# Performance work log

Hardware: AMD Instinct MI355X
Metric: run time of the kernel (lower is better)

The kernel has to match this reference:

```python
import jax, jax.numpy as jnp
import numpy as np

N_NODES = 50000
NUM_HYPEREDGES = 50000


def setup_inputs() -> dict:
    key = jax.random.key(0)
    k1, k2, k3, k4, k5 = jax.random.split(key, 5)
    E = 1_600_000
    F_IN, F_OUT = 128, 128
    X = jax.random.normal(k1, (N_NODES, F_IN), dtype=jnp.float32)
    nodes = jax.random.randint(k2, (E,), 0, N_NODES, dtype=jnp.int64)
    hedges = jax.random.randint(k3, (E,), 0, NUM_HYPEREDGES, dtype=jnp.int64)
    edge_index = jnp.stack([nodes, hedges], axis=0)
    W = jax.random.normal(k4, (F_IN, F_OUT), dtype=jnp.float32) * (1.0 / np.sqrt(F_IN))
    b = jax.random.normal(k5, (F_OUT,), dtype=jnp.float32) * 0.02
    return {"X": X, "edge_index": edge_index, "W": W, "b": b}


def reference(X, edge_index, W, b):
    nodes = edge_index[0]   # [E] node ids (source of incidence)
    hedges = edge_index[1]  # [E] hyperedge ids
    ones = jnp.ones(nodes.shape[0], dtype=X.dtype)

    # x = lin(X)  (Linear, bias=False inside conv)
    x = X @ W  # [N, F_out]

    # B = 1 / hyperedge degree (inf -> 0)
    deg_e = jax.ops.segment_sum(ones, hedges, num_segments=NUM_HYPEREDGES)
    B_inv = jnp.where(deg_e > 0, 1.0 / deg_e, 0.0)

    # D = 1 / node degree (unit hyperedge weights; inf -> 0)
    deg_v = jax.ops.segment_sum(ones, nodes, num_segments=N_NODES)
    D_inv = jnp.where(deg_v > 0, 1.0 / deg_v, 0.0)

    # node -> hyperedge aggregation: m_e = B_e * sum_{v in e} x_v
    m = jax.ops.segment_sum(x[nodes], hedges, num_segments=NUM_HYPEREDGES)
    m = m * B_inv[:, None]  # [M, F_out]

    # hyperedge -> node aggregation: out_v = D_v * sum_{e ni v} m_e
    out = jax.ops.segment_sum(m[hedges], nodes, num_segments=N_NODES)
    out = out * D_inv[:, None] + b  # [N, F_out]

    return jax.nn.softmax(out, axis=1)
```

## Files before the change

### kernel.cpp

```cpp
#include <hip/hip_runtime.h>
#include <hip/hip_fp16.h>

#define NN 50000
#define NM 50000
#define F  128
#define NBUK 782
#define CHSZ 8192
typedef unsigned short ushort_t;
typedef _Float16 f16;
typedef f16 f16x8 __attribute__((ext_vector_type(8)));
typedef float f32x4 __attribute__((ext_vector_type(4)));

union HF4 { float4 f4; __half2 h2[4]; };
union PK4 { uint2 u2; f16 h[4]; };

__device__ __forceinline__ int wscan64(int v, int lane) {
    int x = v;
#pragma unroll
    for (int s = 1; s < 64; s <<= 1) {
        int u = __shfl_up(x, s, 64);
        if (lane >= s) x += u;
    }
    return x;
}

__device__ __forceinline__ int bscan256(int v, int* s5, int* tot) {
    int t = threadIdx.x, lane = t & 63, wid = t >> 6;
    int incl = wscan64(v, lane);
    if (lane == 63) s5[wid] = incl;
    __syncthreads();
    if (t == 0) {
        int a = 0;
#pragma unroll
        for (int j = 0; j < 4; ++j) { int x = s5[j]; s5[j] = a; a += x; }
        s5[4] = a;
    }
    __syncthreads();
    int ex = incl - v + s5[wid];
    *tot = s5[4];
    __syncthreads();
    return ex;
}

__global__ __launch_bounds__(256) void wprep_k(const float* __restrict__ W,
                                               f16* __restrict__ Wt) {
    int i = blockIdx.x * 256 + threadIdx.x;
    int k = i >> 7, c = i & 127;
    Wt[c * 128 + k] = (f16)W[i];
}

struct GemmSmem { f16 sXh[64 * 128]; };
struct SortSmem { int hist[NBUK]; int cursor[NBUK]; int pairs[CHSZ]; int s5[5]; };
union alignas(16) FatSmem { GemmSmem g; SortSmem s; };

__global__ __launch_bounds__(256) void fat_k(const float* __restrict__ X,
                                             const f16* __restrict__ Wt,
                                             f16* __restrict__ xh,
                                             const int* __restrict__ nodes,
                                             const int* __restrict__ hedges,
                                             int* __restrict__ gchunk0, int* __restrict__ gchunk1,
                                             int* __restrict__ ghist, int* __restrict__ gstart,
                                             int E, int NCH, int nsort) {
    __shared__ FatSmem u;
    int t = threadIdx.x;

    if ((int)blockIdx.x < nsort) {
        int dir = blockIdx.x / NCH;
        int c   = blockIdx.x % NCH;
        const int* key = dir ? nodes  : hedges;
        const int* pay = dir ? hedges : nodes;
        int* gchunk    = dir ? gchunk1 : gchunk0;
        int e0 = c * CHSZ, e1 = min(E, e0 + CHSZ);

        for (int i = t; i < NBUK; i += 256) u.s.hist[i] = 0;
        __syncthreads();
        for (int e = e0 + t; e < e1; e += 256) atomicAdd(&u.s.hist[key[e] >> 6], 1);
        __syncthreads();

        int carry = 0;
        for (int base = 0; base < NBUK; base += 256) {
            int i = base + t;
            int v = (i < NBUK) ? u.s.hist[i] : 0;
            int tot;
            int ex = bscan256(v, u.s.s5, &tot);
            if (i < NBUK) u.s.cursor[i] = ex + carry;
            carry += tot;
        }
        __syncthreads();

        for (int b = t; b < NBUK; b += 256) {
            size_t idx = ((size_t)dir * NBUK + b) * NCH + c;
            ghist[idx]  = u.s.hist[b];
            gstart[idx] = u.s.cursor[b];
        }
        __syncthreads();

        for (int e = e0 + t; e < e1; e += 256) {
            int k = key[e];
            int pos = atomicAdd(&u.s.cursor[k >> 6], 1);
            u.s.pairs[pos] = ((k & 63) << 16) | pay[e];
        }
        __syncthreads();

        int n = e1 - e0;
        for (int i = t; i < n; i += 256) gchunk[(size_t)c * CHSZ + i] = u.s.pairs[i];
    } else {
        int gb = blockIdx.x - nsort;
        int row0 = gb * 64;

        const float4* X4 = (const float4*)X;
        for (int i = t; i < 64 * 32; i += 256) {
            int r = i >> 5, cq = i & 31;
            int gr = row0 + r;
            float4 xv = (gr < NN) ? X4[(size_t)gr * 32 + cq]
                                  : make_float4(0.f, 0.f, 0.f, 0.f);
            PK4 pk;
            pk.h[0] = (f16)xv.x; pk.h[1] = (f16)xv.y;
            pk.h[2] = (f16)xv.z; pk.h[3] = (f16)xv.w;
            int byte = (r * 256 + cq * 8) ^ ((r & 7) << 4);
            *(uint2*)((char*)u.g.sXh + byte) = pk.u2;
        }
        __syncthreads();

        int l = t & 63, w = t >> 6;
        int lr = l & 15, lk = l >> 4;
        f32x4 acc[8];
#pragma unroll
        for (int c = 0; c < 8; ++c) acc[c] = (f32x4){0.f, 0.f, 0.f, 0.f};

#pragma unroll
        for (int ks = 0; ks < 4; ++ks) {
            int rloc = w * 16 + lr;
            int abyte = (rloc * 256 + ks * 64 + lk * 16) ^ ((rloc & 7) << 4);
            f16x8 afrag = *(const f16x8*)((const char*)u.g.sXh + abyte);
#pragma unroll
            for (int c = 0; c < 8; ++c) {
                f16x8 bfrag = *(const f16x8*)(Wt + (c * 16 + lr) * 128 + ks * 32 + lk * 8);
                acc[c] = __builtin_amdgcn_mfma_f32_16x16x32_f16(afrag, bfrag, acc[c], 0, 0, 0);
            }
        }

#pragma unroll
        for (int c = 0; c < 8; ++c) {
            int col = c * 16 + lr;
#pragma unroll
            for (int j = 0; j < 4; ++j) {
                int row = row0 + w * 16 + lk * 4 + j;
                if (row < NN) xh[(size_t)row * 128 + col] = (f16)acc[c][j];
            }
        }
    }
}

__global__ __launch_bounds__(256) void rowsum_k(const int* __restrict__ ghist,
                                                int* __restrict__ bsum, int NCH) {
    int row = blockIdx.x * 4 + (threadIdx.x >> 6);
    int l = threadIdx.x & 63;
    if (row >= 2 * NBUK) return;
    const int* r = ghist + (size_t)row * NCH;
    int s = 0;
    for (int c = l; c < NCH; c += 64) s += r[c];
#pragma unroll
    for (int k = 32; k >= 1; k >>= 1) s += __shfl_xor(s, k, 64);
    if (l == 0) bsum[row] = s;
}

__global__ __launch_bounds__(1024) void bucketbase_k(const int* __restrict__ bsum,
                                                     int* __restrict__ bstart,
                                                     int* __restrict__ off0, int* __restrict__ off1,
                                                     int E) {
    __shared__ int s16[17];
    int dir = blockIdx.x;
    int t = threadIdx.x, lane = t & 63, wid = t >> 6;
    int v = (t < NBUK) ? bsum[dir * NBUK + t] : 0;
    int incl = wscan64(v, lane);
    if (lane == 63) s16[wid] = incl;
    __syncthreads();
    if (t < 16) {
        int x = s16[t], y = x;
#pragma unroll
        for (int s = 1; s < 16; s <<= 1) {
            int u = __shfl_up(y, s, 64);
            if (t >= s) y += u;
        }
        s16[t] = y - x;
    }
    __syncthreads();
    int ex = incl - v + s16[wid];
    if (t < NBUK) bstart[dir * NBUK + t] = ex;
    if (t == 0) (dir ? off1 : off0)[50000] = E;
}

__global__ __launch_bounds__(256) void merge_scatter_k(const int* __restrict__ gchunk0, const int* __restrict__ gchunk1,
                                                       const int* __restrict__ ghist, const int* __restrict__ gstart,
                                                       const int* __restrict__ bstart,
                                                       ushort_t* __restrict__ adj0, ushort_t* __restrict__ adj1,
                                                       int* __restrict__ off0, int* __restrict__ off1,
                                                       int NCH) {
    __shared__ int ssrc[256];
    __shared__ int sdst[257];
    __shared__ int s5[5];
    __shared__ int pairsS[CHSZ];
    __shared__ int fcnt[64], foff[64], fcur[64];

    int dir = blockIdx.x / NBUK;
    int b   = blockIdx.x % NBUK;
    int t   = threadIdx.x;
    const int* gchunk   = dir ? gchunk1 : gchunk0;
    ushort_t* adj       = dir ? adj1 : adj0;
    int* offD           = dir ? off1 : off0;

    int len = 0, src = 0;
    if (t < NCH) {
        size_t idx = ((size_t)dir * NBUK + b) * NCH + t;
        len = ghist[idx];
        src = gstart[idx];
    }
    ssrc[t] = src;
    int tot;
    int ex = bscan256(len, s5, &tot);
    sdst[t] = ex;
    if (t == 0) sdst[256] = 0x7FFFFFFF;
    if (t < 64) fcnt[t] = 0;
    __syncthreads();
    int T = tot;

    int per = (T + 255) >> 8;
    int i0 = t * per, i1 = min(T, i0 + per);
    if (i0 < i1) {
        int lo = 0, hi = 255;
        while (lo < hi) {
            int mid = (lo + hi + 1) >> 1;
            if (sdst[mid] <= i0) lo = mid; else hi = mid - 1;
        }
        int c = lo;
        for (int i = i0; i < i1; ++i) {
            while (c < 255 && sdst[c + 1] <= i) ++c;
            int p = gchunk[(size_t)c * CHSZ + ssrc[c] + (i - sdst[c])];
            pairsS[i] = p;
            atomicAdd(&fcnt[p >> 16], 1);
        }
    }
    __syncthreads();

    int bst = bstart[dir * NBUK + b];
    if (t < 64) {
        int x = fcnt[t];
        int y = wscan64(x, t);
        foff[t] = y - x;
        fcur[t] = y - x;
        int d = b * 64 + t;
        if (d < 50000) offD[d] = bst + foff[t];
    }
    __syncthreads();

    for (int i = t; i < T; i += 256) {
        int p = pairsS[i];
        int slot = atomicAdd(&fcur[p >> 16], 1);
        adj[(size_t)bst + slot] = (ushort_t)(p & 0xFFFF);
    }
}

__global__ __launch_bounds__(256) void agg_a_k(const float4* __restrict__ x4,
                                               const ushort_t* __restrict__ adj,
                                               const int* __restrict__ off,
                                               float4* __restrict__ m4) {
    int t = threadIdx.x;
    int seg = blockIdx.x * 4 + (t >> 6);
    int l = t & 63;
    int rg = l >> 4, cc = l & 15;
    int p0 = off[seg], p1 = off[seg + 1];
    float acc[8] = {};
    int i = p0;
    for (; i + 16 <= p1; i += 16) {
        int r0 = adj[i + rg], r1 = adj[i + 4 + rg], r2 = adj[i + 8 + rg], r3 = adj[i + 12 + rg];
        HF4 u0, u1, u2, u3;
        u0.f4 = x4[(size_t)r0 * 16 + cc];
        u1.f4 = x4[(size_t)r1 * 16 + cc];
        u2.f4 = x4[(size_t)r2 * 16 + cc];
        u3.f4 = x4[(size_t)r3 * 16 + cc];
#pragma unroll
        for (int k = 0; k < 4; ++k) {
            float2 f0 = __half22float2(u0.h2[k]);
            float2 f1 = __half22float2(u1.h2[k]);
            float2 f2 = __half22float2(u2.h2[k]);
            float2 f3 = __half22float2(u3.h2[k]);
            acc[2 * k]     += (f0.x + f1.x) + (f2.x + f3.x);
            acc[2 * k + 1] += (f0.y + f1.y) + (f2.y + f3.y);
        }
    }
    for (; i < p1; i += 4) {
        int r = i + rg;
        if (r < p1) {
            HF4 u;
            u.f4 = x4[(size_t)adj[r] * 16 + cc];
#pragma unroll
            for (int k = 0; k < 4; ++k) {
                float2 f = __half22float2(u.h2[k]);
                acc[2 * k] += f.x; acc[2 * k + 1] += f.y;
            }
        }
    }
#pragma unroll
    for (int k = 0; k < 8; ++k) {
        acc[k] += __shfl_xor(acc[k], 16, 64);
        acc[k] += __shfl_xor(acc[k], 32, 64);
    }
    if (l < 16) {
        float inv = (p1 > p0) ? 1.0f / (float)(p1 - p0) : 0.0f;
        HF4 w;
#pragma unroll
        for (int k = 0; k < 4; ++k)
            w.h2[k] = __floats2half2_rn(acc[2 * k] * inv, acc[2 * k + 1] * inv);
        m4[(size_t)seg * 16 + cc] = w.f4;
    }
}

__global__ __launch_bounds__(256) void agg_b_k(const float4* __restrict__ m4,
                                               const ushort_t* __restrict__ adj,
                                               const int* __restrict__ off,
                                               const float* __restrict__ bias,
                                               float4* __restrict__ out4) {
    int t = threadIdx.x;
    int seg = blockIdx.x * 4 + (t >> 6);
    int l = t & 63;
    int rg = l >> 4, cc = l & 15;
    int p0 = off[seg], p1 = off[seg + 1];
    float acc[8] = {};
    int i = p0;
    for (; i + 16 <= p1; i += 16) {
        int r0 = adj[i + rg], r1 = adj[i + 4 + rg], r2 = adj[i + 8 + rg], r3 = adj[i + 12 + rg];
        HF4 u0, u1, u2, u3;
        u0.f4 = m4[(size_t)r0 * 16 + cc];
        u1.f4 = m4[(size_t)r1 * 16 + cc];
        u2.f4 = m4[(size_t)r2 * 16 + cc];
        u3.f4 = m4[(size_t)r3 * 16 + cc];
#pragma unroll
        for (int k = 0; k < 4; ++k) {
            float2 f0 = __half22float2(u0.h2[k]);
            float2 f1 = __half22float2(u1.h2[k]);
            float2 f2 = __half22float2(u2.h2[k]);
            float2 f3 = __half22float2(u3.h2[k]);
            acc[2 * k]     += (f0.x + f1.x) + (f2.x + f3.x);
            acc[2 * k + 1] += (f0.y + f1.y) + (f2.y + f3.y);
        }
    }
    for (; i < p1; i += 4) {
        int r = i + rg;
        if (r < p1) {
            HF4 u;
            u.f4 = m4[(size_t)adj[r] * 16 + cc];
#pragma unroll
            for (int k = 0; k < 4; ++k) {
                float2 f = __half22float2(u.h2[k]);
                acc[2 * k] += f.x; acc[2 * k + 1] += f.y;
            }
        }
    }
#pragma unroll
    for (int k = 0; k < 8; ++k) {
        acc[k] += __shfl_xor(acc[k], 16, 64);
        acc[k] += __shfl_xor(acc[k], 32, 64);
    }
    float inv = (p1 > p0) ? 1.0f / (float)(p1 - p0) : 0.0f;
    const float4* b4 = (const float4*)bias;
    float4 bb0 = b4[cc * 2], bb1 = b4[cc * 2 + 1];
    float lg[8];
    lg[0] = acc[0] * inv + bb0.x; lg[1] = acc[1] * inv + bb0.y;
    lg[2] = acc[2] * inv + bb0.z; lg[3] = acc[3] * inv + bb0.w;
    lg[4] = acc[4] * inv + bb1.x; lg[5] = acc[5] * inv + bb1.y;
    lg[6] = acc[6] * inv + bb1.z; lg[7] = acc[7] * inv + bb1.w;

    float mx = lg[0];
#pragma unroll
    for (int k = 1; k < 8; ++k) mx = fmaxf(mx, lg[k]);
#pragma unroll
    for (int s = 1; s < 16; s <<= 1) mx = fmaxf(mx, __shfl_xor(mx, s, 16));
    float e[8], sm = 0.f;
#pragma unroll
    for (int k = 0; k < 8; ++k) { e[k] = __expf(lg[k] - mx); sm += e[k]; }
#pragma unroll
    for (int s = 1; s < 16; s <<= 1) sm += __shfl_xor(sm, s, 16);
    float r = 1.0f / sm;
    if (l < 16) {
        out4[(size_t)seg * 32 + cc * 2]     = make_float4(e[0] * r, e[1] * r, e[2] * r, e[3] * r);
        out4[(size_t)seg * 32 + cc * 2 + 1] = make_float4(e[4] * r, e[5] * r, e[6] * r, e[7] * r);
    }
}

extern "C" void kernel_launch(void* const* d_in, const int* in_sizes, int n_in,
                              void* d_out, int out_size, void* d_ws, size_t ws_size,
                              hipStream_t stream) {
    const float* X  = (const float*)d_in[0];
    const int*   ei = (const int*)d_in[1];
    const float* W  = (const float*)d_in[2];
    const float* b  = (const float*)d_in[3];

    int E = in_sizes[1] / 2;
    const int* nodes  = ei;
    const int* hedges = ei + E;
    int NCH = (E + CHSZ - 1) / CHSZ;
    int nsort = 2 * NCH;
    int gemmb = (NN + 63) / 64;

    char* p = (char*)d_ws;
    f16* xh = (f16*)p;                    p += (size_t)NN * F * 2;
    f16* mh = (f16*)p;                    p += (size_t)NM * F * 2;
    ushort_t* adj0 = (ushort_t*)p;        p += (size_t)E * 2;
    ushort_t* adj1 = (ushort_t*)p;        p += (size_t)E * 2;
    int* ghist  = (int*)p;                p += (size_t)2 * NBUK * NCH * 4;
    int* gstart = (int*)p;                p += (size_t)2 * NBUK * NCH * 4;
    int* bstart = (int*)p;                p += (size_t)2 * NBUK * 4;
    int* bsum   = (int*)p;                p += (size_t)2 * NBUK * 4;
    int* off0   = (int*)p;                p += (size_t)(NN + 1) * 4;
    int* off1   = (int*)p;                p += (size_t)(NN + 1) * 4;
    f16* Wt     = (f16*)p;                p += (size_t)128 * 128 * 2;
    p = (char*)(((uintptr_t)p + 15) & ~(uintptr_t)15);
    int* gchunk0 = (int*)p;
    int* gchunk1 = gchunk0 + (size_t)NCH * CHSZ;

    wprep_k<<<64, 256, 0, stream>>>(W, Wt);
    fat_k<<<nsort + gemmb, 256, 0, stream>>>(X, Wt, xh, nodes, hedges,
                                             gchunk0, gchunk1, ghist, gstart, E, NCH, nsort);
    rowsum_k<<<(2 * NBUK + 3) / 4, 256, 0, stream>>>(ghist, bsum, NCH);
    bucketbase_k<<<2, 1024, 0, stream>>>(bsum, bstart, off0, off1, E);
    merge_scatter_k<<<2 * NBUK, 256, 0, stream>>>(gchunk0, gchunk1, ghist, gstart, bstart,
                                                  adj0, adj1, off0, off1, NCH);
    agg_a_k<<<NM / 4, 256, 0, stream>>>((const float4*)xh, adj0, off0, (float4*)mh);
    agg_b_k<<<NN / 4, 256, 0, stream>>>((const float4*)mh, adj1, off1, b, (float4*)d_out);
}
```

Before: 182.2 us.

## Halve sort chunk size and accumulate gathers in packed half2 arithmetic

```diff
diff --git a/kernel.cpp b/kernel.cpp
--- a/kernel.cpp
+++ b/kernel.cpp
@@ -5,7 +5,7 @@
 #define NM 50000
 #define F  128
 #define NBUK 782
-#define CHSZ 8192
+#define CHSZ 4096
 typedef unsigned short ushort_t;
 typedef _Float16 f16;
 typedef f16 f16x8 __attribute__((ext_vector_type(8)));
@@ -197,8 +197,8 @@
                                                        ushort_t* __restrict__ adj0, ushort_t* __restrict__ adj1,
                                                        int* __restrict__ off0, int* __restrict__ off1,
                                                        int NCH) {
-    __shared__ int ssrc[256];
-    __shared__ int sdst[257];
+    __shared__ int ssrc[512];
+    __shared__ int sdst[513];
     __shared__ int s5[5];
     __shared__ int pairsS[CHSZ];
     __shared__ int fcnt[64], foff[64], fcur[64];
@@ -210,32 +210,40 @@
     ushort_t* adj       = dir ? adj1 : adj0;
     int* offD           = dir ? off1 : off0;
 
-    int len = 0, src = 0;
+    int len0 = 0, src0 = 0, len1 = 0, src1 = 0;
     if (t < NCH) {
         size_t idx = ((size_t)dir * NBUK + b) * NCH + t;
-        len = ghist[idx];
-        src = gstart[idx];
-    }
-    ssrc[t] = src;
-    int tot;
-    int ex = bscan256(len, s5, &tot);
-    sdst[t] = ex;
-    if (t == 0) sdst[256] = 0x7FFFFFFF;
+        len0 = ghist[idx];
+        src0 = gstart[idx];
+    }
+    if (t + 256 < NCH) {
+        size_t idx = ((size_t)dir * NBUK + b) * NCH + t + 256;
+        len1 = ghist[idx];
+        src1 = gstart[idx];
+    }
+    ssrc[t]       = src0;
+    ssrc[t + 256] = src1;
+    int tot0, tot1;
+    int ex0 = bscan256(len0, s5, &tot0);
+    int ex1 = bscan256(len1, s5, &tot1);
+    sdst[t]       = ex0;
+    sdst[t + 256] = tot0 + ex1;
+    if (t == 0) sdst[512] = tot0 + tot1;
     if (t < 64) fcnt[t] = 0;
     __syncthreads();
-    int T = tot;
+    int T = tot0 + tot1;
 
     int per = (T + 255) >> 8;
     int i0 = t * per, i1 = min(T, i0 + per);
     if (i0 < i1) {
-        int lo = 0, hi = 255;
+        int lo = 0, hi = 511;
         while (lo < hi) {
             int mid = (lo + hi + 1) >> 1;
             if (sdst[mid] <= i0) lo = mid; else hi = mid - 1;
         }
         int c = lo;
         for (int i = i0; i < i1; ++i) {
-            while (c < 255 && sdst[c + 1] <= i) ++c;
+            while (c < 511 && sdst[c + 1] <= i) ++c;
             int p = gchunk[(size_t)c * CHSZ + ssrc[c] + (i - sdst[c])];
             pairsS[i] = p;
             atomicAdd(&fcnt[p >> 16], 1);
@@ -261,62 +269,69 @@
     }
 }
 
-__global__ __launch_bounds__(256) void agg_a_k(const float4* __restrict__ x4,
+__global__ __launch_bounds__(256) void agg_a_k(const char* __restrict__ xb,
                                                const ushort_t* __restrict__ adj,
                                                const int* __restrict__ off,
                                                float4* __restrict__ m4) {
     int t = threadIdx.x;
     int seg = blockIdx.x * 4 + (t >> 6);
     int l = t & 63;
-    int rg = l >> 4, cc = l & 15;
+    int rg = l >> 4;
+    unsigned int cb = (unsigned int)(l & 15) << 4;
     int p0 = off[seg], p1 = off[seg + 1];
-    float acc[8] = {};
+    __half2 z = __floats2half2_rn(0.f, 0.f);
+    __half2 a0 = z, a1 = z, a2 = z, a3 = z;
     int i = p0;
     for (; i + 16 <= p1; i += 16) {
-        int r0 = adj[i + rg], r1 = adj[i + 4 + rg], r2 = adj[i + 8 + rg], r3 = adj[i + 12 + rg];
+        unsigned int o0 = ((unsigned int)adj[i + rg]      << 8) + cb;
+        unsigned int o1 = ((unsigned int)adj[i + 4 + rg]  << 8) + cb;
+        unsigned int o2 = ((unsigned int)adj[i + 8 + rg]  << 8) + cb;
+        unsigned int o3 = ((unsigned int)adj[i + 12 + rg] << 8) + cb;
         HF4 u0, u1, u2, u3;
-        u0.f4 = x4[(size_t)r0 * 16 + cc];
-        u1.f4 = x4[(size_t)r1 * 16 + cc];
-        u2.f4 = x4[(size_t)r2 * 16 + cc];
-        u3.f4 = x4[(size_t)r3 * 16 + cc];
+        u0.f4 = *(const float4*)(xb + o0);
+        u1.f4 = *(const float4*)(xb + o1);
+        u2.f4 = *(const float4*)(xb + o2);
+        u3.f4 = *(const float4*)(xb + o3);
 #pragma unroll
         for (int k = 0; k < 4; ++k) {
-            float2 f0 = __half22float2(u0.h2[k]);
-            float2 f1 = __half22float2(u1.h2[k]);
-            float2 f2 = __half22float2(u2.h2[k]);
-            float2 f3 = __half22float2(u3.h2[k]);
-            acc[2 * k]     += (f0.x + f1.x) + (f2.x + f3.x);
-            acc[2 * k + 1] += (f0.y + f1.y) + (f2.y + f3.y);
+            __half2 s01 = __hadd2(u0.h2[k], u1.h2[k]);
+            __half2 s23 = __hadd2(u2.h2[k], u3.h2[k]);
+            __half2 s = __hadd2(s01, s23);
+            if (k == 0) a0 = __hadd2(a0, s);
+            else if (k == 1) a1 = __hadd2(a1, s);
+            else if (k == 2) a2 = __hadd2(a2, s);
+            else a3 = __hadd2(a3, s);
         }
     }
     for (; i < p1; i += 4) {
         int r = i + rg;
         if (r < p1) {
+            unsigned int o = ((unsigned int)adj[r] << 8) + cb;
             HF4 u;
-            u.f4 = x4[(size_t)adj[r] * 16 + cc];
-#pragma unroll
-            for (int k = 0; k < 4; ++k) {
-                float2 f = __half22float2(u.h2[k]);
-                acc[2 * k] += f.x; acc[2 * k + 1] += f.y;
-            }
-        }
-    }
+            u.f4 = *(const float4*)(xb + o);
+            a0 = __hadd2(a0, u.h2[0]); a1 = __hadd2(a1, u.h2[1]);
+            a2 = __hadd2(a2, u.h2[2]); a3 = __hadd2(a3, u.h2[3]);
+        }
+    }
+    float2 f0 = __half22float2(a0), f1 = __half22float2(a1);
+    float2 f2 = __half22float2(a2), f3 = __half22float2(a3);
+    float v[8] = {f0.x, f0.y, f1.x, f1.y, f2.x, f2.y, f3.x, f3.y};
 #pragma unroll
     for (int k = 0; k < 8; ++k) {
-        acc[k] += __shfl_xor(acc[k], 16, 64);
-        acc[k] += __shfl_xor(acc[k], 32, 64);
+        v[k] += __shfl_xor(v[k], 16, 64);
+        v[k] += __shfl_xor(v[k], 32, 64);
     }
     if (l < 16) {
         float inv = (p1 > p0) ? 1.0f / (float)(p1 - p0) : 0.0f;
         HF4 w;
 #pragma unroll
         for (int k = 0; k < 4; ++k)
-            w.h2[k] = __floats2half2_rn(acc[2 * k] * inv, acc[2 * k + 1] * inv);
-        m4[(size_t)seg * 16 + cc] = w.f4;
-    }
-}
-
-__global__ __launch_bounds__(256) void agg_b_k(const float4* __restrict__ m4,
+            w.h2[k] = __floats2half2_rn(v[2 * k] * inv, v[2 * k + 1] * inv);
+        m4[(size_t)seg * 16 + (l & 15)] = w.f4;
+    }
+}
+
+__global__ __launch_bounds__(256) void agg_b_k(const char* __restrict__ mb,
                                                const ushort_t* __restrict__ adj,
                                                const int* __restrict__ off,
                                                const float* __restrict__ bias,
@@ -324,52 +339,60 @@
     int t = threadIdx.x;
     int seg = blockIdx.x * 4 + (t >> 6);
     int l = t & 63;
-    int rg = l >> 4, cc = l & 15;
+    int rg = l >> 4;
+    int cc = l & 15;
+    unsigned int cb = (unsigned int)cc << 4;
     int p0 = off[seg], p1 = off[seg + 1];
-    float acc[8] = {};
+    __half2 z = __floats2half2_rn(0.f, 0.f);
+    __half2 a0 = z, a1 = z, a2 = z, a3 = z;
     int i = p0;
     for (; i + 16 <= p1; i += 16) {
-        int r0 = adj[i + rg], r1 = adj[i + 4 + rg], r2 = adj[i + 8 + rg], r3 = adj[i + 12 + rg];
+        unsigned int o0 = ((unsigned int)adj[i + rg]      << 8) + cb;
+        unsigned int o1 = ((unsigned int)adj[i + 4 + rg]  << 8) + cb;
+        unsigned int o2 = ((unsigned int)adj[i + 8 + rg]  << 8) + cb;
+        unsigned int o3 = ((unsigned int)adj[i + 12 + rg] << 8) + cb;
         HF4 u0, u1, u2, u3;
-        u0.f4 = m4[(size_t)r0 * 16 + cc];
-        u1.f4 = m4[(size_t)r1 * 16 + cc];
-        u2.f4 = m4[(size_t)r2 * 16 + cc];
-        u3.f4 = m4[(size_t)r3 * 16 + cc];
+        u0.f4 = *(const float4*)(mb + o0);
+        u1.f4 = *(const float4*)(mb + o1);
+        u2.f4 = *(const float4*)(mb + o2);
+        u3.f4 = *(const float4*)(mb + o3);
 #pragma unroll
         for (int k = 0; k < 4; ++k) {
-            float2 f0 = __half22float2(u0.h2[k]);
-            float2 f1 = __half22float2(u1.h2[k]);
-            float2 f2 = __half22float2(u2.h2[k]);
-            float2 f3 = __half22float2(u3.h2[k]);
-            acc[2 * k]     += (f0.x + f1.x) + (f2.x + f3.x);
-            acc[2 * k + 1] += (f0.y + f1.y) + (f2.y + f3.y);
+            __half2 s01 = __hadd2(u0.h2[k], u1.h2[k]);
+            __half2 s23 = __hadd2(u2.h2[k], u3.h2[k]);
+            __half2 s = __hadd2(s01, s23);
+            if (k == 0) a0 = __hadd2(a0, s);
+            else if (k == 1) a1 = __hadd2(a1, s);
+            else if (k == 2) a2 = __hadd2(a2, s);
+            else a3 = __hadd2(a3, s);
         }
     }
     for (; i < p1; i += 4) {
         int r = i + rg;
         if (r < p1) {
+            unsigned int o = ((unsigned int)adj[r] << 8) + cb;
             HF4 u;
-            u.f4 = m4[(size_t)adj[r] * 16 + cc];
-#pragma unroll
-            for (int k = 0; k < 4; ++k) {
-                float2 f = __half22float2(u.h2[k]);
-                acc[2 * k] += f.x; acc[2 * k + 1] += f.y;
-            }
-        }
-    }
+            u.f4 = *(const float4*)(mb + o);
+            a0 = __hadd2(a0, u.h2[0]); a1 = __hadd2(a1, u.h2[1]);
+            a2 = __hadd2(a2, u.h2[2]); a3 = __hadd2(a3, u.h2[3]);
+        }
+    }
+    float2 f0 = __half22float2(a0), f1 = __half22float2(a1);
+    float2 f2 = __half22float2(a2), f3 = __half22float2(a3);
+    float v[8] = {f0.x, f0.y, f1.x, f1.y, f2.x, f2.y, f3.x, f3.y};
 #pragma unroll
     for (int k = 0; k < 8; ++k) {
-        acc[k] += __shfl_xor(acc[k], 16, 64);
-        acc[k] += __shfl_xor(acc[k], 32, 64);
+        v[k] += __shfl_xor(v[k], 16, 64);
+        v[k] += __shfl_xor(v[k], 32, 64);
     }
     float inv = (p1 > p0) ? 1.0f / (float)(p1 - p0) : 0.0f;
     const float4* b4 = (const float4*)bias;
     float4 bb0 = b4[cc * 2], bb1 = b4[cc * 2 + 1];
     float lg[8];
-    lg[0] = acc[0] * inv + bb0.x; lg[1] = acc[1] * inv + bb0.y;
-    lg[2] = acc[2] * inv + bb0.z; lg[3] = acc[3] * inv + bb0.w;
-    lg[4] = acc[4] * inv + bb1.x; lg[5] = acc[5] * inv + bb1.y;
-    lg[6] = acc[6] * inv + bb1.z; lg[7] = acc[7] * inv + bb1.w;
+    lg[0] = v[0] * inv + bb0.x; lg[1] = v[1] * inv + bb0.y;
+    lg[2] = v[2] * inv + bb0.z; lg[3] = v[3] * inv + bb0.w;
+    lg[4] = v[4] * inv + bb1.x; lg[5] = v[5] * inv + bb1.y;
+    lg[6] = v[6] * inv + bb1.z; lg[7] = v[7] * inv + bb1.w;
 
     float mx = lg[0];
 #pragma unroll
@@ -426,6 +449,6 @@
     bucketbase_k<<<2, 1024, 0, stream>>>(bsum, bstart, off0, off1, E);
     merge_scatter_k<<<2 * NBUK, 256, 0, stream>>>(gchunk0, gchunk1, ghist, gstart, bstart,
                                                   adj0, adj1, off0, off1, NCH);
-    agg_a_k<<<NM / 4, 256, 0, stream>>>((const float4*)xh, adj0, off0, (float4*)mh);
-    agg_b_k<<<NN / 4, 256, 0, stream>>>((const float4*)mh, adj1, off1, b, (float4*)d_out);
-}
+    agg_a_k<<<NM / 4, 256, 0, stream>>>((const char*)xh, adj0, off0, (float4*)mh);
+    agg_b_k<<<NN / 4, 256, 0, stream>>>((const char*)mh, adj1, off1, b, (float4*)d_out);
+}
```

New measurement: 213.4 us. +17.1%, slower.
